# Kernel optimization log

Hardware: AMD Instinct MI355X
Metric: run time of the kernel (lower is better)

The kernel has to match this reference:

```python
import jax, jax.numpy as jnp
import numpy as np

B, S, E, H = 4, 1024, 1024, 16
D = E // H  # head dim = 64

def setup_inputs() -> dict:
    key = jax.random.key(0)
    k1, k2, k3, k4, k5 = jax.random.split(key, 5)
    return {
        "lstm_out": jax.random.normal(k1, (B, S, E), dtype=jnp.float32),
        "in_proj_weight": jax.random.normal(k2, (3 * E, E), dtype=jnp.float32) * 0.02,
        "in_proj_bias": jax.random.normal(k3, (3 * E,), dtype=jnp.float32) * 0.02,
        "out_proj_weight": jax.random.normal(k4, (E, E), dtype=jnp.float32) * 0.02,
        "out_proj_bias": jax.random.normal(k5, (E,), dtype=jnp.float32) * 0.02,
    }

def reference(lstm_out, in_proj_weight, in_proj_bias, out_proj_weight, out_proj_bias):
    # Packed QKV projection, as in nn.MultiheadAttention (Linear uses x @ W.T + b)
    qkv = lstm_out @ in_proj_weight.T + in_proj_bias          # [B,S,3E]
    q, k, v = jnp.split(qkv, 3, axis=-1)                      # each [B,S,E]
    def heads(t):
        return t.reshape(B, S, H, D).transpose(0, 2, 1, 3)    # [B,H,S,D]
    q, k, v = heads(q), heads(k), heads(v)
    scale = 1.0 / jnp.sqrt(jnp.asarray(D, dtype=q.dtype))
    scores = jnp.einsum("bhsd,bhtd->bhst", q * scale, k)      # [B,H,S,S]
    attn = jax.nn.softmax(scores, axis=-1)                    # [B,H,S,S]
    ctx = jnp.einsum("bhst,bhtd->bhsd", attn, v)              # [B,H,S,D]
    ctx = ctx.transpose(0, 2, 1, 3).reshape(B, S, E)          # [B,S,E]
    attn_output = ctx @ out_proj_weight.T + out_proj_bias     # [B,S,E]
    # need_weights=True with default average_attn_weights=True -> mean over heads
    attn_weights = attn.mean(axis=1)                          # [B,S,S]
    context_vector = attn_output.mean(axis=1)                 # [B,E]
    return (context_vector, attn_weights)
```

## Files before the change

### kernel.cpp

```cpp
#include <hip/hip_runtime.h>


typedef unsigned short u16;
using s16x8 = __attribute__((ext_vector_type(8))) short;
using f32x4 = __attribute__((ext_vector_type(4))) float;
using u16x4 = __attribute__((ext_vector_type(4))) unsigned short;

#define AS1 __attribute__((address_space(1)))
#define AS3 __attribute__((address_space(3)))

#define QSCALE 0.1803368801111204f

__device__ __forceinline__ u16 f2bf(float f) {
    unsigned u = __float_as_uint(f);
    u += 0x7fffu + ((u >> 16) & 1u);
    return (u16)(u >> 16);
}

__global__ void k_prep(const float* __restrict__ X, const float* __restrict__ W1,
                       const float* __restrict__ W2, const float* __restrict__ bout,
                       u16* __restrict__ Xb, u16* __restrict__ W1b, u16* __restrict__ W2b,
                       float* __restrict__ out) {
    int i = blockIdx.x * blockDim.x + threadIdx.x;
    const float* src; u16* dst; int off;
    if (i < 1048576)       { src = X;  dst = Xb;  off = i; }
    else if (i < 1835008)  { src = W1; dst = W1b; off = i - 1048576; }
    else                   { src = W2; dst = W2b; off = i - 1835008; }
    float4 v = reinterpret_cast<const float4*>(src)[off];
    u16x4 o = { f2bf(v.x), f2bf(v.y), f2bf(v.z), f2bf(v.w) };
    reinterpret_cast<u16x4*>(dst)[off] = o;
    if (i < 4096) out[i] = bout[i & 1023];
}

template<int MODE>
__global__ __launch_bounds__(512) void k_gemm_bt(
    const u16* __restrict__ A, const u16* __restrict__ B,
    const float* __restrict__ bias, u16* __restrict__ C,
    u16* __restrict__ vt, float* __restrict__ outvec) {
    const int K = 1024;
    constexpr int KSLICE = (MODE == 0) ? 1024 : 256;
    const int nbx = gridDim.x;
    const int nwg = nbx * gridDim.y;
    const int bid = blockIdx.y * nbx + blockIdx.x;
    const int per = nwg >> 3;
    const int swz = (bid & 7) * per + (bid >> 3);
    const int n0 = (swz % nbx) * 128, m0 = (swz / nbx) * 128;
    const int kbeg = blockIdx.z * KSLICE, kend = kbeg + KSLICE;
    const int tid = threadIdx.x, lane = tid & 63, w = tid >> 6;
    const int wm = w >> 1, wn = w & 1;
    const int g = lane >> 4, l15 = lane & 15;
    __shared__ __attribute__((aligned(16))) u16 As[2][128 * 64];
    __shared__ __attribute__((aligned(16))) u16 Bs[2][128 * 64];

    f32x4 acc[2][4];
    #pragma unroll
    for (int mi = 0; mi < 2; ++mi)
        #pragma unroll
        for (int nj = 0; nj < 4; ++nj) acc[mi][nj] = (f32x4){0.f, 0.f, 0.f, 0.f};

    auto STAGE = [&](int k0, int sb) {
        #pragma unroll
        for (int r = 0; r < 2; ++r) {
            int c = tid + r * 512;
            int row = c >> 3, j = c & 7;
            int js = j ^ (row & 7);
            __builtin_amdgcn_global_load_lds(
                (AS1 const void*)(A + (size_t)(m0 + row) * K + k0 + js * 8),
                (AS3 void*)(&As[sb][c * 8]), 16, 0, 0);
            __builtin_amdgcn_global_load_lds(
                (AS1 const void*)(B + (size_t)(n0 + row) * K + k0 + js * 8),
                (AS3 void*)(&Bs[sb][c * 8]), 16, 0, 0);
        }
    };

    STAGE(kbeg, 0);
    int buf = 0;
    for (int k0 = kbeg; k0 < kend; k0 += 64) {
        __syncthreads();
        if (k0 + 64 < kend) STAGE(k0 + 64, buf ^ 1);
        #pragma unroll
        for (int kk = 0; kk < 64; kk += 32) {
            const int cx0 = (((kk >> 3) + g) ^ (l15 & 7)) * 8;
            s16x8 av[2], bv[4];
            #pragma unroll
            for (int mi = 0; mi < 2; ++mi)
                av[mi] = *reinterpret_cast<const s16x8*>(
                    &As[buf][(wm * 32 + mi * 16 + l15) * 64 + cx0]);
            #pragma unroll
            for (int nj = 0; nj < 4; ++nj)
                bv[nj] = *reinterpret_cast<const s16x8*>(
                    &Bs[buf][(wn * 64 + nj * 16 + l15) * 64 + cx0]);
            #pragma unroll
            for (int mi = 0; mi < 2; ++mi)
                #pragma unroll
                for (int nj = 0; nj < 4; ++nj)
                    acc[mi][nj] = __builtin_amdgcn_mfma_f32_16x16x32_bf16(av[mi], bv[nj], acc[mi][nj], 0, 0, 0);
        }
        buf ^= 1;
    }

    if constexpr (MODE == 0) {
        #pragma unroll
        for (int nj = 0; nj < 4; ++nj) {
            int n = n0 + wn * 64 + nj * 16 + l15;
            float scale = (n < 1024) ? QSCALE : 1.0f;
            float bvs = bias[n] * scale;
            if (n < 2048) {
                #pragma unroll
                for (int mi = 0; mi < 2; ++mi)
                    #pragma unroll
                    for (int i = 0; i < 4; ++i) {
                        int m = m0 + wm * 32 + mi * 16 + g * 4 + i;
                        C[(size_t)m * 2048 + n] = f2bf(acc[mi][nj][i] * scale + bvs);
                    }
            } else {
                int hd = n - 2048;
                #pragma unroll
                for (int mi = 0; mi < 2; ++mi)
                    #pragma unroll
                    for (int i = 0; i < 4; ++i) {
                        int m = m0 + wm * 32 + mi * 16 + g * 4 + i;
                        int b = m >> 10, t = m & 1023;
                        vt[((size_t)(b * 16 + (hd >> 6)) * 64 + (hd & 63)) * 1024 + t] =
                            f2bf(acc[mi][nj][i] + bvs);
                    }
            }
        }
    } else {
        int b = m0 >> 10;
        #pragma unroll
        for (int nj = 0; nj < 4; ++nj) {
            float s = 0.f;
            #pragma unroll
            for (int mi = 0; mi < 2; ++mi)
                #pragma unroll
                for (int i = 0; i < 4; ++i) s += acc[mi][nj][i];
            s += __shfl_xor(s, 16);
            s += __shfl_xor(s, 32);
            if (g == 0) {
                int n = n0 + wn * 64 + nj * 16 + l15;
                atomicAdd(&outvec[b * 1024 + n], s * (1.0f / 1024.0f));
            }
        }
    }
}

__global__ __launch_bounds__(256, 4) void k_flash(const u16* __restrict__ qk,
                                                  const u16* __restrict__ vt,
                                                  u16* __restrict__ ctx,
                                                  float* __restrict__ ml) {
    const int id = blockIdx.x + 16 * (blockIdx.y + 16 * blockIdx.z);
    const int x = id & 7, kq = id >> 3;
    const int gbh = x * 8 + (kq >> 4);
    const int qt = kq & 15;
    const int b = gbh >> 4, h = gbh & 15;
    const int q0 = qt * 64;
    const int tid = threadIdx.x, lane = tid & 63, w = tid >> 6;
    const int g = lane >> 4, l15 = lane & 15;
    __shared__ __attribute__((aligned(16))) u16 Ks[2][64 * 64];
    __shared__ __attribute__((aligned(16))) u16 Vt[2][64 * 64];
    __shared__ __attribute__((aligned(16))) u16 Ps[4][16 * 64];

    const size_t rowQ = (size_t)(b * 1024 + q0 + w * 16 + l15) * 2048 + h * 64;
    const s16x8 qa0 = *reinterpret_cast<const s16x8*>(qk + rowQ + g * 8);
    const s16x8 qa1 = *reinterpret_cast<const s16x8*>(qk + rowQ + 32 + g * 8);
    const s16x8 onesv = { (short)0x3F80, (short)0x3F80, (short)0x3F80, (short)0x3F80,
                          (short)0x3F80, (short)0x3F80, (short)0x3F80, (short)0x3F80 };

    const int cA = tid, cB = tid + 256;
    const int rowA = cA >> 3, jA = cA & 7, rowB = cB >> 3, jB = cB & 7;
    const u16* kbase0 = qk + (size_t)(b * 1024) * 2048 + 1024 + h * 64;
    const u16* vtb = vt + (size_t)(b * 16 + h) * 65536;

    __builtin_amdgcn_global_load_lds((AS1 const void*)(kbase0 + (size_t)rowA * 2048 + ((jA ^ (rowA & 7)) * 8)),
                                     (AS3 void*)(&Ks[0][cA * 8]), 16, 0, 0);
    __builtin_amdgcn_global_load_lds((AS1 const void*)(kbase0 + (size_t)rowB * 2048 + ((jB ^ (rowB & 7)) * 8)),
                                     (AS3 void*)(&Ks[0][cB * 8]), 16, 0, 0);
    __builtin_amdgcn_global_load_lds((AS1 const void*)(vtb + (size_t)rowA * 1024 + ((jA ^ (rowA & 7)) * 8)),
                                     (AS3 void*)(&Vt[0][cA * 8]), 16, 0, 0);
    __builtin_amdgcn_global_load_lds((AS1 const void*)(vtb + (size_t)rowB * 1024 + ((jB ^ (rowB & 7)) * 8)),
                                     (AS3 void*)(&Vt[0][cB * 8]), 16, 0, 0);

    f32x4 ctxa[4];
    #pragma unroll
    for (int nj = 0; nj < 4; ++nj) ctxa[nj] = (f32x4){0.f, 0.f, 0.f, 0.f};
    f32x4 lacc = (f32x4){0.f, 0.f, 0.f, 0.f};

    int buf = 0;
    for (int kt = 0; kt < 16; ++kt) {
        __syncthreads();
        if (kt < 15) {
            int t0n = (kt + 1) * 64;
            const u16* kbase = kbase0 + (size_t)t0n * 2048;
            __builtin_amdgcn_global_load_lds((AS1 const void*)(kbase + (size_t)rowA * 2048 + ((jA ^ (rowA & 7)) * 8)),
                                             (AS3 void*)(&Ks[buf ^ 1][cA * 8]), 16, 0, 0);
            __builtin_amdgcn_global_load_lds((AS1 const void*)(kbase + (size_t)rowB * 2048 + ((jB ^ (rowB & 7)) * 8)),
                                             (AS3 void*)(&Ks[buf ^ 1][cB * 8]), 16, 0, 0);
            const u16* vbase = vtb + t0n;
            __builtin_amdgcn_global_load_lds((AS1 const void*)(vbase + (size_t)rowA * 1024 + ((jA ^ (rowA & 7)) * 8)),
                                             (AS3 void*)(&Vt[buf ^ 1][cA * 8]), 16, 0, 0);
            __builtin_amdgcn_global_load_lds((AS1 const void*)(vbase + (size_t)rowB * 1024 + ((jB ^ (rowB & 7)) * 8)),
                                             (AS3 void*)(&Vt[buf ^ 1][cB * 8]), 16, 0, 0);
        }

        f32x4 sc[4];
        #pragma unroll
        for (int tj = 0; tj < 4; ++tj) sc[tj] = (f32x4){0.f, 0.f, 0.f, 0.f};
        __builtin_amdgcn_s_setprio(1);
        #pragma unroll
        for (int kk = 0; kk < 64; kk += 32) {
            s16x8 qa = kk ? qa1 : qa0;
            #pragma unroll
            for (int tj = 0; tj < 4; ++tj) {
                int trow = tj * 16 + l15;
                s16x8 kb = *reinterpret_cast<const s16x8*>(
                    &Ks[buf][trow * 64 + ((((kk >> 3) + g) ^ (trow & 7)) * 8)]);
                sc[tj] = __builtin_amdgcn_mfma_f32_16x16x32_bf16(kb, qa, sc[tj], 0, 0, 0);
            }
        }
        __builtin_amdgcn_s_setprio(0);

        #pragma unroll
        for (int tj = 0; tj < 4; ++tj)
            #pragma unroll
            for (int i = 0; i < 4; ++i)
                sc[tj][i] = exp2f(sc[tj][i]);

        #pragma unroll
        for (int tj = 0; tj < 4; ++tj) {
            unsigned pk01, pk23;
            asm("v_cvt_pk_bf16_f32 %0, %1, %2" : "=v"(pk01) : "v"(sc[tj][0]), "v"(sc[tj][1]));
            asm("v_cvt_pk_bf16_f32 %0, %1, %2" : "=v"(pk23) : "v"(sc[tj][2]), "v"(sc[tj][3]));
            uint2 pk = { pk01, pk23 };
            *reinterpret_cast<uint2*>(
                &Ps[w][l15 * 64 + (((tj * 2 + (g >> 1)) ^ (l15 & 7)) * 8) + (g & 1) * 4]) = pk;
        }

        __builtin_amdgcn_s_setprio(1);
        #pragma unroll
        for (int kk = 0; kk < 64; kk += 32) {
            s16x8 pa = *reinterpret_cast<const s16x8*>(
                &Ps[w][l15 * 64 + ((((kk >> 3) + g) ^ (l15 & 7)) * 8)]);
            lacc = __builtin_amdgcn_mfma_f32_16x16x32_bf16(pa, onesv, lacc, 0, 0, 0);
            #pragma unroll
            for (int nj = 0; nj < 4; ++nj) {
                int d = nj * 16 + l15;
                s16x8 vb = *reinterpret_cast<const s16x8*>(
                    &Vt[buf][d * 64 + ((((kk >> 3) + g) ^ (d & 7)) * 8)]);
                ctxa[nj] = __builtin_amdgcn_mfma_f32_16x16x32_bf16(pa, vb, ctxa[nj], 0, 0, 0);
            }
        }
        __builtin_amdgcn_s_setprio(0);
        buf ^= 1;
    }

    #pragma unroll
    for (int i = 0; i < 4; ++i) {
        float invl = 1.0f / lacc[i];
        int row = q0 + w * 16 + g * 4 + i;
        if (l15 == 0)
            ml[(size_t)(b * 16 + h) * 1024 + row] = invl * 0.0625f;
        #pragma unroll
        for (int nj = 0; nj < 4; ++nj) {
            int d = nj * 16 + l15;
            ctx[(size_t)(b * 1024 + row) * 1024 + h * 64 + d] = f2bf(ctxa[nj][i] * invl);
        }
    }
}

__global__ __launch_bounds__(256, 4) void k_attnw(const u16* __restrict__ qk,
                                                  const float* __restrict__ ml,
                                                  float* __restrict__ attnw) {
    const int tt = blockIdx.x, stp = blockIdx.y, b = blockIdx.z;
    const int s0a = stp * 128, t0 = tt * 64;
    const int tid = threadIdx.x, lane = tid & 63, w = tid >> 6;
    const int g = lane >> 4, l15 = lane & 15;
    __shared__ __attribute__((aligned(16))) u16 Ks[2][64 * 64];
    __shared__ float mls[16][128];

    #pragma unroll
    for (int r = 0; r < 8; ++r) {
        int idx = tid + r * 256;
        int hh = idx >> 7, row = idx & 127;
        mls[hh][row] = ml[(size_t)(b * 16 + hh) * 1024 + s0a + row];
    }

    const int cA = tid, cB = tid + 256;
    const int rowA = cA >> 3, jA = cA & 7, rowB = cB >> 3, jB = cB & 7;
    const u16* kbase = qk + (size_t)(b * 1024 + t0) * 2048 + 1024;
    const size_t rowQa = (size_t)(b * 1024 + s0a + w * 16 + l15) * 2048;
    const size_t rowQb = rowQa + (size_t)64 * 2048;

    __builtin_amdgcn_global_load_lds((AS1 const void*)(kbase + (size_t)rowA * 2048 + ((jA ^ (rowA & 7)) * 8)),
                                     (AS3 void*)(&Ks[0][cA * 8]), 16, 0, 0);
    __builtin_amdgcn_global_load_lds((AS1 const void*)(kbase + (size_t)rowB * 2048 + ((jB ^ (rowB & 7)) * 8)),
                                     (AS3 void*)(&Ks[0][cB * 8]), 16, 0, 0);
    s16x8 qcA0 = *reinterpret_cast<const s16x8*>(qk + rowQa + g * 8);
    s16x8 qcA1 = *reinterpret_cast<const s16x8*>(qk + rowQa + 32 + g * 8);
    s16x8 qcB0 = *reinterpret_cast<const s16x8*>(qk + rowQb + g * 8);
    s16x8 qcB1 = *reinterpret_cast<const s16x8*>(qk + rowQb + 32 + g * 8);

    f32x4 accA[4], accB[4];
    #pragma unroll
    for (int tj = 0; tj < 4; ++tj) {
        accA[tj] = (f32x4){0.f, 0.f, 0.f, 0.f};
        accB[tj] = (f32x4){0.f, 0.f, 0.f, 0.f};
    }

    int buf = 0;
    for (int h = 0; h < 16; ++h) {
        __syncthreads();
        s16x8 qnA0, qnA1, qnB0, qnB1;
        if (h < 15) {
            const u16* kb2 = kbase + (h + 1) * 64;
            __builtin_amdgcn_global_load_lds((AS1 const void*)(kb2 + (size_t)rowA * 2048 + ((jA ^ (rowA & 7)) * 8)),
                                             (AS3 void*)(&Ks[buf ^ 1][cA * 8]), 16, 0, 0);
            __builtin_amdgcn_global_load_lds((AS1 const void*)(kb2 + (size_t)rowB * 2048 + ((jB ^ (rowB & 7)) * 8)),
                                             (AS3 void*)(&Ks[buf ^ 1][cB * 8]), 16, 0, 0);
            qnA0 = *reinterpret_cast<const s16x8*>(qk + rowQa + (h + 1) * 64 + g * 8);
            qnA1 = *reinterpret_cast<const s16x8*>(qk + rowQa + (h + 1) * 64 + 32 + g * 8);
            qnB0 = *reinterpret_cast<const s16x8*>(qk + rowQb + (h + 1) * 64 + g * 8);
            qnB1 = *reinterpret_cast<const s16x8*>(qk + rowQb + (h + 1) * 64 + 32 + g * 8);
        }

        f32x4 scA[4], scB[4];
        #pragma unroll
        for (int tj = 0; tj < 4; ++tj) {
            scA[tj] = (f32x4){0.f, 0.f, 0.f, 0.f};
            scB[tj] = (f32x4){0.f, 0.f, 0.f, 0.f};
        }
        #pragma unroll
        for (int kk = 0; kk < 64; kk += 32) {
            s16x8 qaA = kk ? qcA1 : qcA0;
            s16x8 qaB = kk ? qcB1 : qcB0;
            #pragma unroll
            for (int tj = 0; tj < 4; ++tj) {
                int trow = tj * 16 + l15;
                s16x8 kb = *reinterpret_cast<const s16x8*>(
                    &Ks[buf][trow * 64 + ((((kk >> 3) + g) ^ (trow & 7)) * 8)]);
                scA[tj] = __builtin_amdgcn_mfma_f32_16x16x32_bf16(qaA, kb, scA[tj], 0, 0, 0);
                scB[tj] = __builtin_amdgcn_mfma_f32_16x16x32_bf16(qaB, kb, scB[tj], 0, 0, 0);
            }
        }
        #pragma unroll
        for (int i = 0; i < 4; ++i) {
            int row = w * 16 + g * 4 + i;
            float Ma = mls[h][row];
            float Mb = mls[h][64 + row];
            #pragma unroll
            for (int tj = 0; tj < 4; ++tj) {
                accA[tj][i] += exp2f(scA[tj][i]) * Ma;
                accB[tj][i] += exp2f(scB[tj][i]) * Mb;
            }
        }
        qcA0 = qnA0; qcA1 = qnA1; qcB0 = qnB0; qcB1 = qnB1;
        buf ^= 1;
    }

    #pragma unroll
    for (int i = 0; i < 4; ++i) {
        int rowa = s0a + w * 16 + g * 4 + i;
        #pragma unroll
        for (int tj = 0; tj < 4; ++tj) {
            attnw[(size_t)(b * 1024 + rowa) * 1024 + t0 + tj * 16 + l15] = accA[tj][i];
            attnw[(size_t)(b * 1024 + rowa + 64) * 1024 + t0 + tj * 16 + l15] = accB[tj][i];
        }
    }
}

extern "C" void kernel_launch(void* const* d_in, const int* in_sizes, int n_in,
                              void* d_out, int out_size, void* d_ws, size_t ws_size,
                              hipStream_t stream) {
    const float* lstm = (const float*)d_in[0];
    const float* wqkv = (const float*)d_in[1];
    const float* bqkv = (const float*)d_in[2];
    const float* wout = (const float*)d_in[3];
    const float* bout = (const float*)d_in[4];
    float* out = (float*)d_out;

    char* ws = (char*)d_ws;
    u16*   Xbf   = (u16*)(ws);
    u16*   Wqkvb = (u16*)(ws + 8u  * 1024 * 1024);
    u16*   Woutb = (u16*)(ws + 14u * 1024 * 1024);
    u16*   qkbuf = (u16*)(ws + 16u * 1024 * 1024);
    u16*   ctx   = (u16*)(ws + 32u * 1024 * 1024);
    u16*   vtg   = (u16*)(ws + 40u * 1024 * 1024);
    float* ml    = (float*)(ws + 48u * 1024 * 1024);

    k_prep<<<8192, 256, 0, stream>>>(lstm, wqkv, wout, bout, Xbf, Wqkvb, Woutb, out);

    k_gemm_bt<0><<<dim3(24, 32), 512, 0, stream>>>(Xbf, Wqkvb, bqkv, qkbuf, vtg, nullptr);
    k_flash<<<dim3(16, 16, 4), 256, 0, stream>>>(qkbuf, vtg, ctx, ml);
    k_attnw<<<dim3(16, 8, 4), 256, 0, stream>>>(qkbuf, ml, out + 4096);
    k_gemm_bt<1><<<dim3(8, 32, 4), 512, 0, stream>>>(ctx, Woutb, nullptr, nullptr, nullptr, out);
}
```

Baseline: 127.2 us.

## Reduce context over sequence before out-projection, replacing full output GEMM with GEMV

Uses linearity of the output projection: the sequence-mean of ctx is accumulated directly in the flash kernel via shuffles and atomics, then a small fp32 GEMV applies the out-projection weight and bias. This removes the full [4096x1024]x[1024x1024] output GEMM, the bf16 ctx buffer write/read, and the bf16 conversion of the output weight. The trade-off is more atomics in the flash epilogue and a 4-block GEMV kernel that has low parallelism, since each thread reads a full weight row.

```diff
diff --git a/kernel.cpp b/kernel.cpp
--- a/kernel.cpp
+++ b/kernel.cpp
@@ -18,34 +18,29 @@
 }
 
 __global__ void k_prep(const float* __restrict__ X, const float* __restrict__ W1,
-                       const float* __restrict__ W2, const float* __restrict__ bout,
-                       u16* __restrict__ Xb, u16* __restrict__ W1b, u16* __restrict__ W2b,
-                       float* __restrict__ out) {
+                       u16* __restrict__ Xb, u16* __restrict__ W1b,
+                       float* __restrict__ cmean) {
     int i = blockIdx.x * blockDim.x + threadIdx.x;
     const float* src; u16* dst; int off;
     if (i < 1048576)       { src = X;  dst = Xb;  off = i; }
-    else if (i < 1835008)  { src = W1; dst = W1b; off = i - 1048576; }
-    else                   { src = W2; dst = W2b; off = i - 1835008; }
+    else                   { src = W1; dst = W1b; off = i - 1048576; }
     float4 v = reinterpret_cast<const float4*>(src)[off];
     u16x4 o = { f2bf(v.x), f2bf(v.y), f2bf(v.z), f2bf(v.w) };
     reinterpret_cast<u16x4*>(dst)[off] = o;
-    if (i < 4096) out[i] = bout[i & 1023];
-}
-
-template<int MODE>
+    if (i < 4096) cmean[i] = 0.f;
+}
+
 __global__ __launch_bounds__(512) void k_gemm_bt(
     const u16* __restrict__ A, const u16* __restrict__ B,
     const float* __restrict__ bias, u16* __restrict__ C,
-    u16* __restrict__ vt, float* __restrict__ outvec) {
+    u16* __restrict__ vt) {
     const int K = 1024;
-    constexpr int KSLICE = (MODE == 0) ? 1024 : 256;
     const int nbx = gridDim.x;
     const int nwg = nbx * gridDim.y;
     const int bid = blockIdx.y * nbx + blockIdx.x;
     const int per = nwg >> 3;
     const int swz = (bid & 7) * per + (bid >> 3);
     const int n0 = (swz % nbx) * 128, m0 = (swz / nbx) * 128;
-    const int kbeg = blockIdx.z * KSLICE, kend = kbeg + KSLICE;
     const int tid = threadIdx.x, lane = tid & 63, w = tid >> 6;
     const int wm = w >> 1, wn = w & 1;
     const int g = lane >> 4, l15 = lane & 15;
@@ -73,11 +68,11 @@
         }
     };
 
-    STAGE(kbeg, 0);
+    STAGE(0, 0);
     int buf = 0;
-    for (int k0 = kbeg; k0 < kend; k0 += 64) {
+    for (int k0 = 0; k0 < K; k0 += 64) {
         __syncthreads();
-        if (k0 + 64 < kend) STAGE(k0 + 64, buf ^ 1);
+        if (k0 + 64 < K) STAGE(k0 + 64, buf ^ 1);
         #pragma unroll
         for (int kk = 0; kk < 64; kk += 32) {
             const int cx0 = (((kk >> 3) + g) ^ (l15 & 7)) * 8;
@@ -99,56 +94,38 @@
         buf ^= 1;
     }
 
-    if constexpr (MODE == 0) {
-        #pragma unroll
-        for (int nj = 0; nj < 4; ++nj) {
-            int n = n0 + wn * 64 + nj * 16 + l15;
-            float scale = (n < 1024) ? QSCALE : 1.0f;
-            float bvs = bias[n] * scale;
-            if (n < 2048) {
-                #pragma unroll
-                for (int mi = 0; mi < 2; ++mi)
-                    #pragma unroll
-                    for (int i = 0; i < 4; ++i) {
-                        int m = m0 + wm * 32 + mi * 16 + g * 4 + i;
-                        C[(size_t)m * 2048 + n] = f2bf(acc[mi][nj][i] * scale + bvs);
-                    }
-            } else {
-                int hd = n - 2048;
-                #pragma unroll
-                for (int mi = 0; mi < 2; ++mi)
-                    #pragma unroll
-                    for (int i = 0; i < 4; ++i) {
-                        int m = m0 + wm * 32 + mi * 16 + g * 4 + i;
-                        int b = m >> 10, t = m & 1023;
-                        vt[((size_t)(b * 16 + (hd >> 6)) * 64 + (hd & 63)) * 1024 + t] =
-                            f2bf(acc[mi][nj][i] + bvs);
-                    }
-            }
-        }
-    } else {
-        int b = m0 >> 10;
-        #pragma unroll
-        for (int nj = 0; nj < 4; ++nj) {
-            float s = 0.f;
+    #pragma unroll
+    for (int nj = 0; nj < 4; ++nj) {
+        int n = n0 + wn * 64 + nj * 16 + l15;
+        float scale = (n < 1024) ? QSCALE : 1.0f;
+        float bvs = bias[n] * scale;
+        if (n < 2048) {
             #pragma unroll
             for (int mi = 0; mi < 2; ++mi)
                 #pragma unroll
-                for (int i = 0; i < 4; ++i) s += acc[mi][nj][i];
-            s += __shfl_xor(s, 16);
-            s += __shfl_xor(s, 32);
-            if (g == 0) {
-                int n = n0 + wn * 64 + nj * 16 + l15;
-                atomicAdd(&outvec[b * 1024 + n], s * (1.0f / 1024.0f));
-            }
+                for (int i = 0; i < 4; ++i) {
+                    int m = m0 + wm * 32 + mi * 16 + g * 4 + i;
+                    C[(size_t)m * 2048 + n] = f2bf(acc[mi][nj][i] * scale + bvs);
+                }
+        } else {
+            int hd = n - 2048;
+            #pragma unroll
+            for (int mi = 0; mi < 2; ++mi)
+                #pragma unroll
+                for (int i = 0; i < 4; ++i) {
+                    int m = m0 + wm * 32 + mi * 16 + g * 4 + i;
+                    int b = m >> 10, t = m & 1023;
+                    vt[((size_t)(b * 16 + (hd >> 6)) * 64 + (hd & 63)) * 1024 + t] =
+                        f2bf(acc[mi][nj][i] + bvs);
+                }
         }
     }
 }
 
 __global__ __launch_bounds__(256, 4) void k_flash(const u16* __restrict__ qk,
                                                   const u16* __restrict__ vt,
-                                                  u16* __restrict__ ctx,
-                                                  float* __restrict__ ml) {
+                                                  float* __restrict__ ml,
+                                                  float* __restrict__ cmean) {
     const int id = blockIdx.x + 16 * (blockIdx.y + 16 * blockIdx.z);
     const int x = id & 7, kq = id >> 3;
     const int gbh = x * 8 + (kq >> 4);
@@ -254,17 +231,22 @@
         buf ^= 1;
     }
 
+    float inv_i[4];
     #pragma unroll
     for (int i = 0; i < 4; ++i) {
-        float invl = 1.0f / lacc[i];
-        int row = q0 + w * 16 + g * 4 + i;
+        inv_i[i] = 1.0f / lacc[i];
         if (l15 == 0)
-            ml[(size_t)(b * 16 + h) * 1024 + row] = invl * 0.0625f;
-        #pragma unroll
-        for (int nj = 0; nj < 4; ++nj) {
-            int d = nj * 16 + l15;
-            ctx[(size_t)(b * 1024 + row) * 1024 + h * 64 + d] = f2bf(ctxa[nj][i] * invl);
-        }
+            ml[(size_t)(b * 16 + h) * 1024 + q0 + w * 16 + g * 4 + i] = inv_i[i] * 0.0625f;
+    }
+
+    #pragma unroll
+    for (int nj = 0; nj < 4; ++nj) {
+        float s = ctxa[nj][0] * inv_i[0] + ctxa[nj][1] * inv_i[1]
+                + ctxa[nj][2] * inv_i[2] + ctxa[nj][3] * inv_i[3];
+        s += __shfl_xor(s, 16);
+        s += __shfl_xor(s, 32);
+        if (g == 0)
+            atomicAdd(&cmean[b * 1024 + h * 64 + nj * 16 + l15], s * (1.0f / 1024.0f));
     }
 }
 
@@ -368,6 +350,39 @@
     }
 }
 
+__global__ __launch_bounds__(256) void k_outproj(const float* __restrict__ cmean,
+                                                 const float* __restrict__ wout,
+                                                 const float* __restrict__ bias,
+                                                 float* __restrict__ out) {
+    __shared__ float cs[4096];
+    #pragma unroll
+    for (int r = 0; r < 16; ++r) {
+        int idx = threadIdx.x + r * 256;
+        cs[idx] = cmean[idx];
+    }
+    __syncthreads();
+    int e = blockIdx.x * 256 + threadIdx.x;
+    const float4* wr = reinterpret_cast<const float4*>(wout) + (size_t)e * 256;
+    const float4* c0 = reinterpret_cast<const float4*>(&cs[0]);
+    const float4* c1 = reinterpret_cast<const float4*>(&cs[1024]);
+    const float4* c2 = reinterpret_cast<const float4*>(&cs[2048]);
+    const float4* c3 = reinterpret_cast<const float4*>(&cs[3072]);
+    float s0 = 0.f, s1 = 0.f, s2 = 0.f, s3 = 0.f;
+    for (int k = 0; k < 256; ++k) {
+        float4 wv = wr[k];
+        float4 a = c0[k], b = c1[k], c = c2[k], d = c3[k];
+        s0 += a.x * wv.x + a.y * wv.y + a.z * wv.z + a.w * wv.w;
+        s1 += b.x * wv.x + b.y * wv.y + b.z * wv.z + b.w * wv.w;
+        s2 += c.x * wv.x + c.y * wv.y + c.z * wv.z + c.w * wv.w;
+        s3 += d.x * wv.x + d.y * wv.y + d.z * wv.z + d.w * wv.w;
+    }
+    float bv = bias[e];
+    out[e]        = s0 + bv;
+    out[1024 + e] = s1 + bv;
+    out[2048 + e] = s2 + bv;
+    out[3072 + e] = s3 + bv;
+}
+
 extern "C" void kernel_launch(void* const* d_in, const int* in_sizes, int n_in,
                               void* d_out, int out_size, void* d_ws, size_t ws_size,
                               hipStream_t stream) {
@@ -381,16 +396,15 @@
     char* ws = (char*)d_ws;
     u16*   Xbf   = (u16*)(ws);
     u16*   Wqkvb = (u16*)(ws + 8u  * 1024 * 1024);
-    u16*   Woutb = (u16*)(ws + 14u * 1024 * 1024);
     u16*   qkbuf = (u16*)(ws + 16u * 1024 * 1024);
-    u16*   ctx   = (u16*)(ws + 32u * 1024 * 1024);
-    u16*   vtg   = (u16*)(ws + 40u * 1024 * 1024);
-    float* ml    = (float*)(ws + 48u * 1024 * 1024);
-
-    k_prep<<<8192, 256, 0, stream>>>(lstm, wqkv, wout, bout, Xbf, Wqkvb, Woutb, out);
-
-    k_gemm_bt<0><<<dim3(24, 32), 512, 0, stream>>>(Xbf, Wqkvb, bqkv, qkbuf, vtg, nullptr);
-    k_flash<<<dim3(16, 16, 4), 256, 0, stream>>>(qkbuf, vtg, ctx, ml);
+    u16*   vtg   = (u16*)(ws + 32u * 1024 * 1024);
+    float* ml    = (float*)(ws + 40u * 1024 * 1024);
+    float* cmean = (float*)(ws + 41u * 1024 * 1024);
+
+    k_prep<<<7168, 256, 0, stream>>>(lstm, wqkv, Xbf, Wqkvb, cmean);
+
+    k_gemm_bt<<<dim3(24, 32), 512, 0, stream>>>(Xbf, Wqkvb, bqkv, qkbuf, vtg);
+    k_flash<<<dim3(16, 16, 4), 256, 0, stream>>>(qkbuf, vtg, ml, cmean);
     k_attnw<<<dim3(16, 8, 4), 256, 0, stream>>>(qkbuf, ml, out + 4096);
-    k_gemm_bt<1><<<dim3(8, 32, 4), 512, 0, stream>>>(ctx, Woutb, nullptr, nullptr, nullptr, out);
-}
+    k_outproj<<<4, 256, 0, stream>>>(cmean, wout, bout, out);
+}
```

Result: slower. 153.6 us (+20.8%).
